# Kernel tuning notes

Hardware: AMD Instinct MI355X
Metric: run time of the kernel (lower is better)

## Reference

```python
import jax, jax.numpy as jnp
import numpy as np

NUM_CAPSULE = 32
DIM_VECTOR = 16
NUM_ROUTING = 3

def squash(v, axis=-1):
    s2 = jnp.sum(jnp.square(v), axis=axis, keepdims=True)
    scale = s2 / (1.0 + s2) / jnp.sqrt(s2)
    return scale * v

def setup_inputs() -> dict:
    key = jax.random.key(0)
    k1, k2 = jax.random.split(key)
    B, IN_CAPS, IN_DIM = 64, 2048, 8
    x = jax.random.normal(k1, (B, IN_CAPS, IN_DIM), dtype=jnp.float32)
    # glorot-uniform-ish weight: [in_caps, num_caps, in_dim, out_dim]
    limit = np.sqrt(6.0 / (IN_DIM + DIM_VECTOR)).astype(np.float32)
    W = jax.random.uniform(k2, (IN_CAPS, NUM_CAPSULE, IN_DIM, DIM_VECTOR), dtype=jnp.float32, minval=-limit, maxval=limit)
    return {"x": x, "W": W}

def reference(x, W):
    # x: [B, in_caps, in_dim]; W: [in_caps, num_caps, in_dim, out_dim]
    # inputs_hat (u_hat): [B, in_caps, num_caps, out_dim]
    u_hat = jnp.einsum('bid,inde->bine', x, W)
    B, IN_CAPS = u_hat.shape[0], u_hat.shape[1]
    # routing logits; original broadcasts over out_dim with identical values,
    # so a trailing singleton dim is mathematically equivalent
    b = jnp.zeros((B, IN_CAPS, NUM_CAPSULE, 1), dtype=u_hat.dtype)
    v = None
    for i in range(NUM_ROUTING):
        c = jax.nn.softmax(b, axis=2)                       # over num_capsule
        s = jnp.sum(c * u_hat, axis=1, keepdims=True)       # [B,1,nc,out]
        v = squash(s)                                       # [B,1,nc,out]
        if i != NUM_ROUTING - 1:
            b = b + jnp.sum(u_hat * v, axis=-1, keepdims=True)
    return v.reshape(-1, NUM_CAPSULE, DIM_VECTOR)
```

## Files before the change

kernel.cpp:

```cpp
#include <hip/hip_runtime.h>
#include <math.h>


#define B_TOT 64
#define I_TOT 2048
#define D_IN  8
#define NC    32
#define EV    16
#define OD    (NC*EV)
#define BC    8
#define NBC   (B_TOT/BC)
#define ICH   16
#define NIC   (I_TOT/ICH)

__device__ __forceinline__ void fma4(float4& acc, float a, const float4& w) {
    acc.x = fmaf(a, w.x, acc.x);
    acc.y = fmaf(a, w.y, acc.y);
    acc.z = fmaf(a, w.z, acc.z);
    acc.w = fmaf(a, w.w, acc.w);
}

template <int MODE>
__global__ __launch_bounds__(256, 4)
void route_pass(const float* __restrict__ x, const float* __restrict__ W,
                float* __restrict__ P, const float* __restrict__ vin,
                float* __restrict__ aws)
{
    __shared__ __align__(16) float xl[BC * ICH * D_IN];
    __shared__ float wsum[2][4][BC];

    const int t  = threadIdx.x;
    const int ic = blockIdx.x & (NIC - 1);
    const int bc = blockIdx.x >> 7;
    const int b0 = bc * BC;
    const int i0 = ic * ICH;
    const int eq = t & 3;
    const int bh = (t >> 2) & 1;
    const int n  = t >> 3;
    const int w  = t >> 6;

    {
        const int row = t >> 5, f = (t & 31) * 4;
        *(float4*)&xl[row * (ICH * D_IN) + f] =
            *(const float4*)&x[((size_t)(b0 + row) * I_TOT + i0) * D_IN + f];
    }

    float4 vr[4];
    if (MODE >= 1) {
        #pragma unroll
        for (int q = 0; q < 4; ++q)
            vr[q] = *(const float4*)&vin[(size_t)(b0 + bh * 4 + q) * OD + n * EV + eq * 4];
    }
    __syncthreads();

    float4 sacc[4];
    #pragma unroll
    for (int q = 0; q < 4; ++q) sacc[q] = make_float4(0.f, 0.f, 0.f, 0.f);

    const float* Wt = &W[(size_t)i0 * 4096 + n * 128 + eq * 4];

    for (int ii = 0; ii < ICH; ++ii) {
        float4 wr[8];
        #pragma unroll
        for (int d = 0; d < 8; ++d)
            wr[d] = *(const float4*)&Wt[ii * 4096 + d * 16];

        float4 u[4];
        #pragma unroll
        for (int q = 0; q < 4; ++q) {
            const int bl = bh * 4 + q;
            float4 xa = *(float4*)&xl[bl * (ICH * D_IN) + ii * 8];
            float4 xb = *(float4*)&xl[bl * (ICH * D_IN) + ii * 8 + 4];
            float4 uu = make_float4(0.f, 0.f, 0.f, 0.f);
            fma4(uu, xa.x, wr[0]); fma4(uu, xa.y, wr[1]);
            fma4(uu, xa.z, wr[2]); fma4(uu, xa.w, wr[3]);
            fma4(uu, xb.x, wr[4]); fma4(uu, xb.y, wr[5]);
            fma4(uu, xb.z, wr[6]); fma4(uu, xb.w, wr[7]);
            u[q] = uu;
        }

        if (MODE == 0) {
            #pragma unroll
            for (int q = 0; q < 4; ++q) {
                sacc[q].x += u[q].x; sacc[q].y += u[q].y;
                sacc[q].z += u[q].z; sacc[q].w += u[q].w;
            }
        } else {
            float a[4];
            #pragma unroll
            for (int q = 0; q < 4; ++q) {
                float ap = u[q].x * vr[q].x + u[q].y * vr[q].y
                         + u[q].z * vr[q].z + u[q].w * vr[q].w;
                ap += __shfl_xor(ap, 1, 64);
                ap += __shfl_xor(ap, 2, 64);
                a[q] = ap;
            }
            const size_t aoff = (((size_t)(i0 + ii) * NBC + bc) * NC + n) * 8 + bh * 4;
            if (MODE == 2) {
                float4 a0 = *(const float4*)&aws[aoff];
                a[0] += a0.x; a[1] += a0.y; a[2] += a0.z; a[3] += a0.w;
            }
            if (MODE == 1 && eq == 0) {
                float4 st = make_float4(a[0], a[1], a[2], a[3]);
                *(float4*)&aws[aoff] = st;
            }
            float e[4], p[4];
            #pragma unroll
            for (int q = 0; q < 4; ++q) {
                e[q] = __expf(a[q]);
                float pp = e[q];
                pp += __shfl_xor(pp, 8, 64);
                pp += __shfl_xor(pp, 16, 64);
                pp += __shfl_xor(pp, 32, 64);
                p[q] = pp;
            }
            if (eq == 0) {
                #pragma unroll
                for (int q = 0; q < 4; ++q)
                    wsum[ii & 1][w][bh * 4 + q] = p[q];
            }
            __syncthreads();
            #pragma unroll
            for (int q = 0; q < 4; ++q) {
                const int bl = bh * 4 + q;
                float s = wsum[ii & 1][0][bl] + wsum[ii & 1][1][bl]
                        + wsum[ii & 1][2][bl] + wsum[ii & 1][3][bl];
                float c = e[q] / s;
                fma4(sacc[q], c, u[q]);
            }
        }
    }

    #pragma unroll
    for (int q = 0; q < 4; ++q)
        *(float4*)&P[((size_t)ic * B_TOT + b0 + bh * 4 + q) * OD + n * EV + eq * 4] = sacc[q];
}

__global__ __launch_bounds__(256, 4)
void reduce_squash(const float* __restrict__ P, float* __restrict__ dst, float pre)
{
    const int b = blockIdx.x;
    const int t = threadIdx.x;
    float s1 = 0.f, s2 = 0.f;
    for (int ic = 0; ic < NIC; ++ic) {
        const float* p = &P[((size_t)ic * B_TOT + b) * OD];
        s1 += p[t];
        s2 += p[t + 256];
    }
    s1 *= pre; s2 *= pre;
    float q1 = s1 * s1, q2 = s2 * s2;
    q1 += __shfl_xor(q1, 1, 64);  q2 += __shfl_xor(q2, 1, 64);
    q1 += __shfl_xor(q1, 2, 64);  q2 += __shfl_xor(q2, 2, 64);
    q1 += __shfl_xor(q1, 4, 64);  q2 += __shfl_xor(q2, 4, 64);
    q1 += __shfl_xor(q1, 8, 64);  q2 += __shfl_xor(q2, 8, 64);
    float sc1 = q1 / ((1.0f + q1) * sqrtf(q1));
    float sc2 = q2 / ((1.0f + q2) * sqrtf(q2));
    dst[b * OD + t]       = s1 * sc1;
    dst[b * OD + t + 256] = s2 * sc2;
}

extern "C" void kernel_launch(void* const* d_in, const int* in_sizes, int n_in,
                              void* d_out, int out_size, void* d_ws, size_t ws_size,
                              hipStream_t stream) {
    const float* x = (const float*)d_in[0];
    const float* W = (const float*)d_in[1];
    float* out = (float*)d_out;

    char* ws = (char*)d_ws;
    float* P   = (float*)ws;
    float* aws = (float*)(ws + (size_t)16 * 1024 * 1024);
    float* v0  = (float*)(ws + (size_t)32 * 1024 * 1024);
    float* v1  = v0 + B_TOT * OD;

    dim3 grid(NBC * NIC), blk(256);

    route_pass<0><<<grid, blk, 0, stream>>>(x, W, P, nullptr, nullptr);
    reduce_squash<<<B_TOT, 256, 0, stream>>>(P, v0, 1.0f / 32.0f);
    route_pass<1><<<grid, blk, 0, stream>>>(x, W, P, v0, aws);
    reduce_squash<<<B_TOT, 256, 0, stream>>>(P, v1, 1.0f);
    route_pass<2><<<grid, blk, 0, stream>>>(x, W, P, v1, aws);
    reduce_squash<<<B_TOT, 256, 0, stream>>>(P, out, 1.0f);
}
```

Before: 198.4 us.

## Fold routing logits via v0+v1 linearity, halve input chunk, parallelize reduction

Because the routing logits are linear in v, the third pass now uses the summed vector v0+v1 and recomputes its dot product directly. This removes the logits workspace that pass two wrote and pass three read back. The input-capsule chunk is halved, doubling the route grid, and the launch-bounds occupancy hint is raised. The reduce/squash kernel is split across 8 blocks per batch row with a shared-memory partial sum, where before one block per row looped serially. The trade-off is that the partial-sum buffer P doubles in size, so the reduction reads more data.

```diff
diff --git a/kernel.cpp b/kernel.cpp
--- a/kernel.cpp
+++ b/kernel.cpp
@@ -10,7 +10,7 @@
 #define OD    (NC*EV)
 #define BC    8
 #define NBC   (B_TOT/BC)
-#define ICH   16
+#define ICH   8
 #define NIC   (I_TOT/ICH)
 
 __device__ __forceinline__ void fma4(float4& acc, float a, const float4& w) {
@@ -21,17 +21,16 @@
 }
 
 template <int MODE>
-__global__ __launch_bounds__(256, 4)
+__global__ __launch_bounds__(256, 8)
 void route_pass(const float* __restrict__ x, const float* __restrict__ W,
-                float* __restrict__ P, const float* __restrict__ vin,
-                float* __restrict__ aws)
+                float* __restrict__ P, const float* __restrict__ vin)
 {
     __shared__ __align__(16) float xl[BC * ICH * D_IN];
     __shared__ float wsum[2][4][BC];
 
     const int t  = threadIdx.x;
     const int ic = blockIdx.x & (NIC - 1);
-    const int bc = blockIdx.x >> 7;
+    const int bc = blockIdx.x >> 8;
     const int b0 = bc * BC;
     const int i0 = ic * ICH;
     const int eq = t & 3;
@@ -39,14 +38,14 @@
     const int n  = t >> 3;
     const int w  = t >> 6;
 
-    {
-        const int row = t >> 5, f = (t & 31) * 4;
+    if (t < 128) {
+        const int row = t >> 4, f = (t & 15) * 4;
         *(float4*)&xl[row * (ICH * D_IN) + f] =
             *(const float4*)&x[((size_t)(b0 + row) * I_TOT + i0) * D_IN + f];
     }
 
     float4 vr[4];
-    if (MODE >= 1) {
+    if (MODE == 1) {
         #pragma unroll
         for (int q = 0; q < 4; ++q)
             vr[q] = *(const float4*)&vin[(size_t)(b0 + bh * 4 + q) * OD + n * EV + eq * 4];
@@ -95,15 +94,6 @@
                 ap += __shfl_xor(ap, 2, 64);
                 a[q] = ap;
             }
-            const size_t aoff = (((size_t)(i0 + ii) * NBC + bc) * NC + n) * 8 + bh * 4;
-            if (MODE == 2) {
-                float4 a0 = *(const float4*)&aws[aoff];
-                a[0] += a0.x; a[1] += a0.y; a[2] += a0.z; a[3] += a0.w;
-            }
-            if (MODE == 1 && eq == 0) {
-                float4 st = make_float4(a[0], a[1], a[2], a[3]);
-                *(float4*)&aws[aoff] = st;
-            }
             float e[4], p[4];
             #pragma unroll
             for (int q = 0; q < 4; ++q) {
@@ -136,27 +126,38 @@
         *(float4*)&P[((size_t)ic * B_TOT + b0 + bh * 4 + q) * OD + n * EV + eq * 4] = sacc[q];
 }
 
-__global__ __launch_bounds__(256, 4)
-void reduce_squash(const float* __restrict__ P, float* __restrict__ dst, float pre)
+__global__ __launch_bounds__(256, 8)
+void reduce_squash(const float* __restrict__ P, float* __restrict__ dst,
+                   const float* __restrict__ addsrc, float pre)
 {
-    const int b = blockIdx.x;
-    const int t = threadIdx.x;
-    float s1 = 0.f, s2 = 0.f;
-    for (int ic = 0; ic < NIC; ++ic) {
-        const float* p = &P[((size_t)ic * B_TOT + b) * OD];
-        s1 += p[t];
-        s2 += p[t + 256];
+    __shared__ float red[256];
+    const int b   = blockIdx.x >> 3;
+    const int oq  = blockIdx.x & 7;
+    const int t   = threadIdx.x;
+    const int o   = oq * 64 + (t & 63);
+    const int icq = t >> 6;
+    const size_t stride = (size_t)B_TOT * OD;
+
+    float s = 0.f;
+    size_t base = ((size_t)(icq * 64) * B_TOT + b) * OD + o;
+    #pragma unroll 8
+    for (int k = 0; k < 64; ++k) s += P[base + (size_t)k * stride];
+    red[t] = s;
+    __syncthreads();
+
+    if (t < 64) {
+        float v = red[t] + red[t + 64] + red[t + 128] + red[t + 192];
+        v *= pre;
+        float q2 = v * v;
+        q2 += __shfl_xor(q2, 1, 64);
+        q2 += __shfl_xor(q2, 2, 64);
+        q2 += __shfl_xor(q2, 4, 64);
+        q2 += __shfl_xor(q2, 8, 64);
+        float sc = q2 / ((1.0f + q2) * sqrtf(q2));
+        float outv = v * sc;
+        if (addsrc) outv += addsrc[b * OD + o];
+        dst[b * OD + o] = outv;
     }
-    s1 *= pre; s2 *= pre;
-    float q1 = s1 * s1, q2 = s2 * s2;
-    q1 += __shfl_xor(q1, 1, 64);  q2 += __shfl_xor(q2, 1, 64);
-    q1 += __shfl_xor(q1, 2, 64);  q2 += __shfl_xor(q2, 2, 64);
-    q1 += __shfl_xor(q1, 4, 64);  q2 += __shfl_xor(q2, 4, 64);
-    q1 += __shfl_xor(q1, 8, 64);  q2 += __shfl_xor(q2, 8, 64);
-    float sc1 = q1 / ((1.0f + q1) * sqrtf(q1));
-    float sc2 = q2 / ((1.0f + q2) * sqrtf(q2));
-    dst[b * OD + t]       = s1 * sc1;
-    dst[b * OD + t + 256] = s2 * sc2;
 }
 
 extern "C" void kernel_launch(void* const* d_in, const int* in_sizes, int n_in,
@@ -167,17 +168,17 @@
     float* out = (float*)d_out;
 
     char* ws = (char*)d_ws;
-    float* P   = (float*)ws;
-    float* aws = (float*)(ws + (size_t)16 * 1024 * 1024);
-    float* v0  = (float*)(ws + (size_t)32 * 1024 * 1024);
-    float* v1  = v0 + B_TOT * OD;
+    float* P  = (float*)ws;
+    float* v0 = (float*)(ws + (size_t)32 * 1024 * 1024);
+    float* vs = v0 + B_TOT * OD;
 
-    dim3 grid(NBC * NIC), blk(256);
+    dim3 rg(NBC * NIC), rb(256);
+    dim3 sg(B_TOT * 8), sb(256);
 
-    route_pass<0><<<grid, blk, 0, stream>>>(x, W, P, nullptr, nullptr);
-    reduce_squash<<<B_TOT, 256, 0, stream>>>(P, v0, 1.0f / 32.0f);
-    route_pass<1><<<grid, blk, 0, stream>>>(x, W, P, v0, aws);
-    reduce_squash<<<B_TOT, 256, 0, stream>>>(P, v1, 1.0f);
-    route_pass<2><<<grid, blk, 0, stream>>>(x, W, P, v1, aws);
-    reduce_squash<<<B_TOT, 256, 0, stream>>>(P, out, 1.0f);
+    route_pass<0><<<rg, rb, 0, stream>>>(x, W, P, nullptr);
+    reduce_squash<<<sg, sb, 0, stream>>>(P, v0, nullptr, 1.0f / 32.0f);
+    route_pass<1><<<rg, rb, 0, stream>>>(x, W, P, v0);
+    reduce_squash<<<sg, sb, 0, stream>>>(P, vs, v0, 1.0f);
+    route_pass<1><<<rg, rb, 0, stream>>>(x, W, P, vs);
+    reduce_squash<<<sg, sb, 0, stream>>>(P, out, nullptr, 1.0f);
 }
```

Measured after the change: 681.6 us. 244% more time.
